# Kernel optimization log

Hardware: AMD Instinct MI355X
Metric: run time of the kernel (lower is better)

The kernel has to match this reference:

```python
import jax, jax.numpy as jnp
import numpy as np

B, T, U, V = 8, 128, 64, 1024
BLANK = V - 1  # blank=-1 resolves to last class index


def setup_inputs() -> dict:
    key = jax.random.key(0)
    k1, k2, k3, k4 = jax.random.split(key, 4)
    logits = jax.random.normal(k1, (B, T, U + 1, V), dtype=jnp.float32)
    targets = jax.random.randint(k2, (B, U), 0, V - 1, dtype=jnp.int32)  # exclude blank
    logit_lengths = jax.random.randint(k3, (B,), T // 2, T + 1, dtype=jnp.int32)
    target_lengths = jax.random.randint(k4, (B,), U // 2, U + 1, dtype=jnp.int32)
    return {
        "logits": logits,
        "targets": targets,
        "logit_lengths": logit_lengths,
        "target_lengths": target_lengths,
    }


def _rnnt_neglogp(logits, targets, logit_lengths, target_lengths, blank):
    """RNNT forward-variable DP (Graves 2012). Returns per-sample -log p(y|x)."""
    Bn, Tn, U1, Vn = logits.shape
    Un = U1 - 1
    lp = jax.nn.log_softmax(logits, axis=-1)  # fused_log_softmax=True
    lp_blank = lp[..., blank]                                  # (B, T, U+1)
    idx = jnp.broadcast_to(targets[:, None, :, None], (Bn, Tn, Un, 1))
    lp_emit = jnp.take_along_axis(lp[:, :, :Un, :], idx, axis=-1)[..., 0]  # (B, T, U)

    # alpha[t, u]: log-prob of emitting first u labels using first t frames.
    # alpha[0, u] = sum_{v<u} emit(0, v)
    row0 = jnp.concatenate(
        [jnp.zeros((Bn, 1), lp.dtype), jnp.cumsum(lp_emit[:, 0, :], axis=-1)], axis=1
    )  # (B, U+1)

    def inner(a_prev, x):
        # a[u] = logaddexp(alpha[t-1,u] + blank(t-1,u),  a[u-1] + emit(t,u-1))
        b_u, e_u = x
        a_new = jnp.logaddexp(b_u, a_prev + e_u)
        return a_new, a_new

    def outer(prev_row, x):
        blank_prev, emit_t = x  # (B, U+1), (B, U)
        b_term = prev_row + blank_prev  # vertical (blank) transition term
        _, rest = jax.lax.scan(
            inner, b_term[:, 0], (b_term[:, 1:].T, emit_t.T)
        )  # rest: (U, B)
        new_row = jnp.concatenate([b_term[:, :1], rest.T], axis=1)  # (B, U+1)
        return new_row, new_row

    xs = (
        jnp.swapaxes(lp_blank[:, :-1, :], 0, 1),  # (T-1, B, U+1)
        jnp.swapaxes(lp_emit[:, 1:, :], 0, 1),    # (T-1, B, U)
    )
    _, rows = jax.lax.scan(outer, row0, xs)
    alpha = jnp.concatenate([row0[None], rows], axis=0)  # (T, B, U+1)

    bidx = jnp.arange(Bn)
    t_last = logit_lengths - 1
    u_last = target_lengths
    a_end = alpha[t_last, bidx, u_last]
    final_blank = lp_blank[bidx, t_last, u_last]
    return -(a_end + final_blank)


def reference(logits, targets, logit_lengths, target_lengths):
    return _rnnt_neglogp(logits, targets, logit_lengths, target_lengths, BLANK)
```

## Files before the change

### kernel.cpp

```cpp
#include <hip/hip_runtime.h>
#include <hip/hip_bf16.h>

#define BB 8
#define TT 128
#define UU 64
#define VV 1024
#define U1 65
#define NROWS (BB * TT * U1)
#define NDIAG (TT + UU)
#define DSZ (NDIAG * U1)
#define QPB (TT * U1)
#define NPROD (NROWS / 4)
#define KPF 4

typedef unsigned long long ull;

__device__ __forceinline__ float wave_sum64(float v) {
#pragma unroll
    for (int off = 32; off; off >>= 1) v += __shfl_xor(v, off, 64);
    return v;
}

__device__ __forceinline__ float2 ldP(const ull* Pb, int idx) {
    union { ull u; float2 f; } c;
    c.u = __hip_atomic_load(Pb + idx, __ATOMIC_RELAXED, __HIP_MEMORY_SCOPE_AGENT);
    return c.f;
}

__device__ __forceinline__ int diag_need(int c) {
    return min(c, 64) - max(0, c - 127) + 1;
}

__device__ __forceinline__ void wait_diag(const unsigned int* cb, int c) {
    const int nd = diag_need(c);
    int guard = 0;
    while ((int)__hip_atomic_load(cb + c, __ATOMIC_RELAXED,
                                  __HIP_MEMORY_SCOPE_AGENT) < nd) {
        __builtin_amdgcn_s_sleep(1);
        if (++guard > (1 << 21)) break;
    }
}

__global__ __launch_bounds__(256) void rnnt_fused_kernel(
    const float* __restrict__ logits, const int* __restrict__ targets,
    const int* __restrict__ logit_lengths, const int* __restrict__ target_lengths,
    ull* __restrict__ P, unsigned int* __restrict__ cnt,
    float* __restrict__ out) {

    if (blockIdx.x < NPROD) {
        const int wave = threadIdx.x >> 6;
        const int lane = threadIdx.x & 63;
        const int r = blockIdx.x * 4 + wave;
        const int b = r & 7;
        const int q = r >> 3;

        int d, j;
        if (q < 2080) {
            d = (int)((__builtin_sqrtf(8.f * q + 1.f) - 1.f) * 0.5f);
            while ((d + 1) * (d + 2) / 2 <= q) ++d;
            while (d * (d + 1) / 2 > q) --d;
            j = q - d * (d + 1) / 2;
        } else if (q < 6240) {
            const int e = q - 2080;
            d = 64 + e / 65;
            j = e - (d - 64) * 65;
        } else {
            const int e = 8319 - q;
            int k = (int)((__builtin_sqrtf(8.f * e + 1.f) - 1.f) * 0.5f);
            while ((k + 1) * (k + 2) / 2 <= e) ++k;
            while (k * (k + 1) / 2 > e) --k;
            d = 191 - k;
            j = k - (e - k * (k + 1) / 2);
        }
        const int u = max(0, d - 127) + j;
        const int t = d - u;

        const float4* p4 =
            (const float4*)(logits + (size_t)((b * TT + t) * U1 + u) * VV);
        float4 x0 = p4[lane];
        float4 x1 = p4[lane + 64];
        float4 x2 = p4[lane + 128];
        float4 x3 = p4[lane + 192];

        float s = __expf(x0.x) + __expf(x0.y) + __expf(x0.z) + __expf(x0.w)
                + __expf(x1.x) + __expf(x1.y) + __expf(x1.z) + __expf(x1.w)
                + __expf(x2.x) + __expf(x2.y) + __expf(x2.z) + __expf(x2.w)
                + __expf(x3.x) + __expf(x3.y) + __expf(x3.z) + __expf(x3.w);
        s = wave_sum64(s);
        const float lse = __logf(s);

        const float blankv = __shfl(x3.w, 63, 64) - lse;
        float emitv = 0.f;
        if (u < UU) {
            const int tgt = targets[b * UU + u];
            const int qq = tgt >> 2, grp = qq >> 6, sl = qq & 63, c4 = tgt & 3;
            float4 g4 = (grp == 0) ? x0 : (grp == 1) ? x1 : (grp == 2) ? x2 : x3;
            float cv = (c4 == 0) ? g4.x : (c4 == 1) ? g4.y : (c4 == 2) ? g4.z : g4.w;
            emitv = __shfl(cv, sl, 64) - lse;
        }
        if (lane == 0) {
            union { ull u; float2 f; } pk;
            pk.f = make_float2(blankv, emitv);
            __hip_atomic_store(P + (size_t)b * DSZ + d * U1 + u, pk.u,
                               __ATOMIC_RELAXED, __HIP_MEMORY_SCOPE_AGENT);
            asm volatile("s_waitcnt vmcnt(0)" ::: "memory");
            __hip_atomic_fetch_add(cnt + b * NDIAG + d, 1u,
                                   __ATOMIC_RELAXED, __HIP_MEMORY_SCOPE_AGENT);
        }
        return;
    }

    if (threadIdx.x >= 64) return;
    const int b = blockIdx.x - NPROD;
    const int l = threadIdx.x;
    const ull* Pb = P + (size_t)b * DSZ;
    const unsigned int* cb = cnt + b * NDIAG;
    const int tl = logit_lengths[b] - 1;
    const int ul = target_lengths[b];
    const int Dfin = tl + ul;

    const float NEG = -1e30f;
    float aprev   = (l == 0) ? 0.f : NEG;
    float aprev64 = NEG;
    float res = 0.f;

    float2 ring[KPF], ring64[KPF];
#pragma unroll
    for (int k = 0; k < KPF; ++k) {
        wait_diag(cb, k);
        ring[k]   = ldP(Pb, k * U1 + l);
        ring64[k] = ldP(Pb, k * U1 + 64);
    }

    for (int base = 1; base <= NDIAG - 1; base += KPF) {
#pragma unroll
        for (int s = 0; s < KPF; ++s) {
            const int d = base + s;
            if (d > NDIAG - 1) break;
            float2 pr   = ring[s];
            float2 p64v = ring64[s];
            float edl = __shfl_up(pr.y, 1, 64);
            float al  = __shfl_up(aprev, 1, 64);
            const int t = d - l;
            float va = (t >= 1) ? aprev + pr.x : NEG;
            float vb = (l >= 1) ? al + edl : NEG;
            float mm = fmaxf(va, vb);
            float r  = mm + __logf(__expf(va - mm) + __expf(vb - mm));
            r = (t >= 0 && t < TT) ? r : NEG;
            const int t64 = d - 64;
            float va64 = (t64 >= 1) ? aprev64 + p64v.x : NEG;
            float vb64 = aprev + pr.y;
            float mm64 = fmaxf(va64, vb64);
            float r64  = mm64 + __logf(__expf(va64 - mm64) + __expf(vb64 - mm64));
            r64 = (t64 >= 0) ? r64 : NEG;
            if (d == Dfin) {
                if (ul < 64) { if (l == ul) res = r; }
                else if (l == 63) res = r64;
            }
            aprev = r; aprev64 = r64;
            const int c2 = d - 1 + KPF;
            if (c2 <= NDIAG - 2) {
                wait_diag(cb, c2);
                ring[s]   = ldP(Pb, c2 * U1 + l);
                ring64[s] = ldP(Pb, c2 * U1 + 64);
            }
        }
    }

    const float rr = __shfl(res, (ul < 64) ? ul : 63, 64);
    if (l == 0) {
        wait_diag(cb, Dfin);
        out[b] = -(rr + ldP(Pb, Dfin * U1 + ul).x);
    }
}

extern "C" void kernel_launch(void* const* d_in, const int* in_sizes, int n_in,
                              void* d_out, int out_size, void* d_ws, size_t ws_size,
                              hipStream_t stream) {
    const float* logits         = (const float*)d_in[0];
    const int*   targets        = (const int*)d_in[1];
    const int*   logit_lengths  = (const int*)d_in[2];
    const int*   target_lengths = (const int*)d_in[3];
    float* outp = (float*)d_out;

    ull* P = (ull*)d_ws;
    unsigned int* cnt = (unsigned int*)((char*)d_ws + (1 << 20));

    hipMemsetAsync(cnt, 0, BB * NDIAG * sizeof(unsigned int), stream);
    rnnt_fused_kernel<<<NPROD + BB, 256, 0, stream>>>(
        logits, targets, logit_lengths, target_lengths, P, cnt, outp);
}
```

Baseline: 492.2 us.

## Launch DP consumer blocks first and map producer rows linearly in memory order

```diff
diff --git a/kernel.cpp b/kernel.cpp
--- a/kernel.cpp
+++ b/kernel.cpp
@@ -9,9 +9,8 @@
 #define NROWS (BB * TT * U1)
 #define NDIAG (TT + UU)
 #define DSZ (NDIAG * U1)
-#define QPB (TT * U1)
 #define NPROD (NROWS / 4)
-#define KPF 4
+#define KPF 8
 
 typedef unsigned long long ull;
 
@@ -37,7 +36,7 @@
     while ((int)__hip_atomic_load(cb + c, __ATOMIC_RELAXED,
                                   __HIP_MEMORY_SCOPE_AGENT) < nd) {
         __builtin_amdgcn_s_sleep(1);
-        if (++guard > (1 << 21)) break;
+        if (++guard > (1 << 22)) break;
     }
 }
 
@@ -47,36 +46,16 @@
     ull* __restrict__ P, unsigned int* __restrict__ cnt,
     float* __restrict__ out) {
 
-    if (blockIdx.x < NPROD) {
+    if (blockIdx.x >= BB) {
         const int wave = threadIdx.x >> 6;
         const int lane = threadIdx.x & 63;
-        const int r = blockIdx.x * 4 + wave;
-        const int b = r & 7;
-        const int q = r >> 3;
+        const int row  = (blockIdx.x - BB) * 4 + wave;
+        const int b   = row / (TT * U1);
+        const int rem = row - b * (TT * U1);
+        const int t   = rem / U1;
+        const int u   = rem - t * U1;
 
-        int d, j;
-        if (q < 2080) {
-            d = (int)((__builtin_sqrtf(8.f * q + 1.f) - 1.f) * 0.5f);
-            while ((d + 1) * (d + 2) / 2 <= q) ++d;
-            while (d * (d + 1) / 2 > q) --d;
-            j = q - d * (d + 1) / 2;
-        } else if (q < 6240) {
-            const int e = q - 2080;
-            d = 64 + e / 65;
-            j = e - (d - 64) * 65;
-        } else {
-            const int e = 8319 - q;
-            int k = (int)((__builtin_sqrtf(8.f * e + 1.f) - 1.f) * 0.5f);
-            while ((k + 1) * (k + 2) / 2 <= e) ++k;
-            while (k * (k + 1) / 2 > e) --k;
-            d = 191 - k;
-            j = k - (e - k * (k + 1) / 2);
-        }
-        const int u = max(0, d - 127) + j;
-        const int t = d - u;
-
-        const float4* p4 =
-            (const float4*)(logits + (size_t)((b * TT + t) * U1 + u) * VV);
+        const float4* p4 = (const float4*)(logits + (size_t)row * VV);
         float4 x0 = p4[lane];
         float4 x1 = p4[lane + 64];
         float4 x2 = p4[lane + 128];
@@ -101,6 +80,7 @@
         if (lane == 0) {
             union { ull u; float2 f; } pk;
             pk.f = make_float2(blankv, emitv);
+            const int d = t + u;
             __hip_atomic_store(P + (size_t)b * DSZ + d * U1 + u, pk.u,
                                __ATOMIC_RELAXED, __HIP_MEMORY_SCOPE_AGENT);
             asm volatile("s_waitcnt vmcnt(0)" ::: "memory");
@@ -111,7 +91,7 @@
     }
 
     if (threadIdx.x >= 64) return;
-    const int b = blockIdx.x - NPROD;
+    const int b = blockIdx.x;
     const int l = threadIdx.x;
     const ull* Pb = P + (size_t)b * DSZ;
     const unsigned int* cb = cnt + b * NDIAG;
@@ -187,6 +167,6 @@
     unsigned int* cnt = (unsigned int*)((char*)d_ws + (1 << 20));
 
     hipMemsetAsync(cnt, 0, BB * NDIAG * sizeof(unsigned int), stream);
-    rnnt_fused_kernel<<<NPROD + BB, 256, 0, stream>>>(
+    rnnt_fused_kernel<<<BB + NPROD, 256, 0, stream>>>(
         logits, targets, logit_lengths, target_lengths, P, cnt, outp);
 }
```

Result: faster. 470.3 us (-4.5%).
